# Kernel tuning notes

Measured on AMD Instinct MI355X. Metric: run time of the kernel, lower is better.

Reference implementation:

```python
import jax, jax.numpy as jnp
import numpy as np

E = 384        # number of edges
HID = 128      # hidden_dim
NH = 8         # num_heads
DH = HID // NH # head_dim = 16
NR = 64        # num_radial
CUTOFF = 10.0
AIN = 2 * DH + NR + 1  # attention MLP input dim = 97


def _xavier(key, fan_in, fan_out):
    a = np.sqrt(6.0 / (fan_in + fan_out))
    return jax.random.uniform(key, (fan_in, fan_out), jnp.float32, -a, a)


def setup_inputs() -> dict:
    key = jax.random.key(0)
    ks = jax.random.split(key, 16)
    return {
        "edge_features": jax.random.normal(ks[0], (E, HID), jnp.float32),
        "edge_coords": jax.random.normal(ks[1], (E, 3), jnp.float32),
        "edge_mask": jnp.zeros((E, E), jnp.float32),  # 0 = connected
        "wq": _xavier(ks[2], HID, HID),
        "wk": _xavier(ks[3], HID, HID),
        "wv": _xavier(ks[4], HID, HID),
        "rbf_centers": jnp.linspace(0.0, CUTOFF, NR).astype(jnp.float32),
        "rbf_widths": jnp.full((NR,), 0.5, jnp.float32),
        "a_w1": _xavier(ks[5], AIN, HID), "a_b1": jnp.zeros((HID,), jnp.float32),
        "a_w2": _xavier(ks[6], HID, HID), "a_b2": jnp.zeros((HID,), jnp.float32),
        "a_w3": _xavier(ks[7], HID, NH),  "a_b3": jnp.zeros((NH,), jnp.float32),
        "g_w1": _xavier(ks[8], DH, HID),  "g_b1": jnp.zeros((HID,), jnp.float32),
        "g_w2": _xavier(ks[9], HID, 1),   "g_b2": jnp.zeros((1,), jnp.float32),
        "wo": _xavier(ks[10], HID, HID),  "bo": jnp.zeros((HID,), jnp.float32),
        "ln_g": jnp.ones((HID,), jnp.float32),
        "ln_b": jnp.zeros((HID,), jnp.float32),
        "edge_index": jax.random.randint(ks[11], (2, E), 0, E, jnp.int64) if jax.config.jax_enable_x64 else jax.random.randint(ks[11], (2, E), 0, E, jnp.int32),
    }


def reference(edge_features, edge_coords, edge_mask,
              wq, wk, wv, rbf_centers, rbf_widths,
              a_w1, a_b1, a_w2, a_b2, a_w3, a_b3,
              g_w1, g_b1, g_w2, g_b2, wo, bo, ln_g, ln_b,
              edge_index):
    silu = jax.nn.silu
    n = edge_features.shape[0]

    q = (edge_features @ wq).reshape(n, NH, DH)
    k = (edge_features @ wk).reshape(n, NH, DH)
    v = (edge_features @ wv).reshape(n, NH, DH)

    # pairwise geometry [E, E, ...]
    coord_diff = edge_coords[:, None, :] - edge_coords[None, :, :]
    dist = jnp.linalg.norm(coord_diff, axis=-1) + 1e-8
    dist = jnp.clip(dist, 1e-8, 1e8)
    dot = jnp.clip(jnp.sum(edge_coords[:, None, :] * edge_coords[None, :, :], -1),
                   -1e8, 1e8)
    d = dist[..., None]                               # [E, E, 1]
    rbf = jnp.exp(-rbf_widths * (d - rbf_centers) ** 2) * (d <= CUTOFF).astype(jnp.float32)

    feats = []
    coords = edge_coords
    for h in range(NH):  # structural loop over fixed num_heads
        qh = jnp.broadcast_to(q[:, h, None, :], (n, n, DH))
        kh = jnp.broadcast_to(k[None, :, h, :], (n, n, DH))
        ai = jnp.concatenate([qh, kh, rbf, dot[..., None]], -1)  # [E, E, 97]
        x = silu(ai @ a_w1 + a_b1)
        x = silu(x @ a_w2 + a_b2)
        scores = (x @ a_w3 + a_b3)[:, :, h] + edge_mask
        scores = jnp.clip(scores, -1e9, 1e9)
        attn = jax.nn.softmax(scores, axis=-1)
        attn = jnp.nan_to_num(attn, nan=0.0, posinf=1.0, neginf=0.0)
        vh = v[:, h, :]
        feats.append(attn @ vh)
        # coord gate from v_head of the query edge, broadcast over keys
        gates = jax.nn.sigmoid(silu(vh @ g_w1 + g_b1) @ g_w2 + g_b2)  # [E, 1]
        coords = coords + jnp.einsum('ij,ijc->ic', attn * gates, coord_diff) / NH

    upd = jnp.concatenate(feats, -1)             # [E, hidden]
    y = edge_features + upd @ wo + bo            # residual + out_proj
    mu = jnp.mean(y, -1, keepdims=True)
    var = jnp.var(y, -1, keepdims=True)
    out_f = (y - mu) / jnp.sqrt(var + 1e-5) * ln_g + ln_b
    return out_f, coords
```

## Files before the change

kernel.cpp:

```cpp
#include <hip/hip_runtime.h>
#include <hip/hip_bf16.h>

#define N 384
#define HIDN 128
#define NHD 8
#define DHD 16
#define NRB 64
#define CUTF 10.0f

#define WS_V 0
#define WS_QPB (WS_V + N*HIDN)
#define WS_KPB (WS_QPB + N*NHD*HIDN/2)
#define WS_GATE (WS_KPB + N*NHD*HIDN/2)
#define WS_UPD (WS_GATE + N*NHD)
#define WS_SCORES (WS_UPD + N*HIDN)

typedef short bf16x8 __attribute__((ext_vector_type(8)));
typedef float floatx4 __attribute__((ext_vector_type(4)));
#define MFMA16(a, b, c) __builtin_amdgcn_mfma_f32_16x16x32_bf16(a, b, c, 0, 0, 0)

__device__ __forceinline__ float siluf(float x) { return x / (1.0f + __expf(-x)); }
__device__ __forceinline__ float silu_fast(float x) {
    return x * __builtin_amdgcn_rcpf(1.0f + __expf(-x));
}
__device__ __forceinline__ short f2bf(float f) {
    unsigned int b = __float_as_uint(f);
    unsigned int r = (b + 0x7fffu + ((b >> 16) & 1u)) >> 16;
    return (short)r;
}
__device__ __forceinline__ float bf2f(short s) {
    return __uint_as_float(((unsigned int)(unsigned short)s) << 16);
}
__device__ __forceinline__ float wave_sum(float v) {
    for (int o = 32; o; o >>= 1) v += __shfl_down(v, o, 64);
    return v;
}

__global__ __launch_bounds__(128) void k_pre(const float* __restrict__ ef,
    const float* __restrict__ wq, const float* __restrict__ wk, const float* __restrict__ wv,
    const float* __restrict__ aw1,
    const float* __restrict__ gw1, const float* __restrict__ gb1,
    const float* __restrict__ gw2, const float* __restrict__ gb2,
    float* __restrict__ v, unsigned short* __restrict__ Qpb,
    unsigned short* __restrict__ Kpb, float* __restrict__ gates) {
    __shared__ float sE[HIDN], sQ[HIDN], sK[HIDN], sV[HIDN];
    __shared__ float sRed[2];
    int i = blockIdx.x, t = threadIdx.x;
    sE[t] = ef[i * HIDN + t];
    __syncthreads();
    float aq = 0.f, ak = 0.f, av = 0.f;
#pragma unroll 8
    for (int c = 0; c < HIDN; c++) {
        float e = sE[c];
        aq += e * wq[c * HIDN + t];
        ak += e * wk[c * HIDN + t];
        av += e * wv[c * HIDN + t];
    }
    v[i * HIDN + t] = av;
    sQ[t] = aq; sK[t] = ak; sV[t] = av;
    __syncthreads();
    for (int h = 0; h < NHD; h++) {
        float accq = 0.f, acck = 0.f;
#pragma unroll
        for (int d = 0; d < DHD; d++) {
            accq += sQ[h * DHD + d] * aw1[d * HIDN + t];
            acck += sK[h * DHD + d] * aw1[(DHD + d) * HIDN + t];
        }
        Qpb[(i * NHD + h) * HIDN + t] = (unsigned short)f2bf(accq);
        Kpb[(i * NHD + h) * HIDN + t] = (unsigned short)f2bf(acck);
        float tt = gb1[t];
#pragma unroll
        for (int d = 0; d < DHD; d++) tt += sV[h * DHD + d] * gw1[d * HIDN + t];
        float contrib = siluf(tt) * gw2[t];
        float s = wave_sum(contrib);
        if ((t & 63) == 0) sRed[t >> 6] = s;
        __syncthreads();
        if (t == 0) gates[i * NHD + h] = 1.0f / (1.0f + __expf(-(sRed[0] + sRed[1] + gb2[0])));
        __syncthreads();
    }
}

#define OFF_W1RT 0
#define OFF_QPB  18432
#define OFF_W3T  20480
#define OFF_B1   24576
#define OFF_W1D  25088
#define OFF_B2   25600
#define OFF_AB3  26112
#define OFF_SDD  26144
#define OFF_RBF  26272
#define OFF_R    28576
#define SMEM_SZ  37024
#define OFF_STAGE 0

__global__ __launch_bounds__(256, 2) void k_scores_mfma(
    const float* __restrict__ coords, const float* __restrict__ mask,
    const float* __restrict__ centers, const float* __restrict__ widths,
    const float* __restrict__ aw1, const float* __restrict__ ab1,
    const float* __restrict__ aw2, const float* __restrict__ ab2,
    const float* __restrict__ aw3, const float* __restrict__ ab3,
    const unsigned short* __restrict__ Qpb, const unsigned short* __restrict__ Kpb,
    float* __restrict__ scores) {
    __shared__ __align__(16) char smem[SMEM_SZ];
    const int t = threadIdx.x;
    const int lane = t & 63;
    const int w = t >> 6;
    const int l15 = lane & 15;
    const int quad = lane >> 4;
    const int i = blockIdx.y;
    const int jb = blockIdx.x * 128;

    for (int idx = t; idx < HIDN * HIDN; idx += 256) {
        int k = idx >> 7, n = idx & 127;
        *(short*)(smem + OFF_STAGE + n * 272 + k * 2) = f2bf(aw2[idx]);
    }
    __syncthreads();
    bf16x8 BW2[8][4];
#pragma unroll
    for (int ct = 0; ct < 8; ct++)
#pragma unroll
        for (int ks = 0; ks < 4; ks++)
            BW2[ct][ks] = *(const bf16x8*)(smem + OFF_STAGE + (ct * 16 + l15) * 272 + ks * 64 + quad * 16);
    __syncthreads();
    for (int idx = t; idx < NRB * HIDN; idx += 256) {
        int r = idx >> 7, n = idx & 127;
        *(short*)(smem + OFF_W1RT + n * 144 + r * 2) = f2bf(aw1[32 * HIDN + idx]);
    }
    {
        const unsigned int* qsrc = (const unsigned int*)(Qpb + (size_t)i * NHD * HIDN);
        for (int idx = t; idx < 512; idx += 256) *(unsigned int*)(smem + OFF_QPB + idx * 4) = qsrc[idx];
    }
    for (int idx = t; idx < HIDN * NHD; idx += 256) {
        int c = idx >> 3, h = idx & 7;
        *(float*)(smem + OFF_W3T + (h * 128 + c) * 4) = aw3[idx];
    }
    if (t < 128) {
        *(float*)(smem + OFF_B1 + t * 4) = ab1[t];
        *(float*)(smem + OFF_W1D + t * 4) = aw1[96 * HIDN + t];
        *(float*)(smem + OFF_B2 + t * 4) = ab2[t];
    }
    if (t < 8) *(float*)(smem + OFF_AB3 + t * 4) = ab3[t];
    const float cix = coords[i * 3], ciy = coords[i * 3 + 1], ciz = coords[i * 3 + 2];
    __syncthreads();

    for (int ch = 0; ch < 8; ch++) {
        const int j0 = jb + ch * 16;
        {
            int r = t & 63, j4 = t >> 6;
            float cr = centers[r], rw = widths[r];
#pragma unroll
            for (int p = 0; p < 4; p++) {
                int j = j4 + p * 4;
                int jj = j0 + j;
                float jx = coords[jj * 3], jy = coords[jj * 3 + 1], jz = coords[jj * 3 + 2];
                float dx = cix - jx, dy = ciy - jy, dz = ciz - jz;
                float dist = sqrtf(dx * dx + dy * dy + dz * dz) + 1e-8f;
                dist = fminf(fmaxf(dist, 1e-8f), 1e8f);
                float dd = dist - cr;
                float val = (dist <= CUTF) ? __expf(-rw * dd * dd) : 0.0f;
                *(short*)(smem + OFF_RBF + j * 144 + r * 2) = f2bf(val);
            }
            if (t < 16) {
                int jj = j0 + t;
                float jx = coords[jj * 3], jy = coords[jj * 3 + 1], jz = coords[jj * 3 + 2];
                float dot = fminf(fmaxf(cix * jx + ciy * jy + ciz * jz, -1e8f), 1e8f);
                *(float*)(smem + OFF_SDD + t * 4) = dot;
            }
        }
        __syncthreads();
        {
            bf16x8 ra0 = *(const bf16x8*)(smem + OFF_RBF + l15 * 144 + quad * 16);
            bf16x8 ra1 = *(const bf16x8*)(smem + OFF_RBF + l15 * 144 + 64 + quad * 16);
#pragma unroll
            for (int cc = 0; cc < 2; cc++) {
                int ct = w + cc * 4;
                floatx4 acc = {0.f, 0.f, 0.f, 0.f};
                bf16x8 b0 = *(const bf16x8*)(smem + OFF_W1RT + (ct * 16 + l15) * 144 + quad * 16);
                bf16x8 b1f = *(const bf16x8*)(smem + OFF_W1RT + (ct * 16 + l15) * 144 + 64 + quad * 16);
                acc = MFMA16(ra0, b0, acc);
                acc = MFMA16(ra1, b1f, acc);
                int c = ct * 16 + l15;
                float b1v = *(const float*)(smem + OFF_B1 + c * 4);
                float w1dv = *(const float*)(smem + OFF_W1D + c * 4);
#pragma unroll
                for (int r = 0; r < 4; r++) {
                    int j = quad * 4 + r;
                    float dotv = *(const float*)(smem + OFF_SDD + j * 4);
                    *(float*)(smem + OFF_R + j * 528 + c * 4) = acc[r] + b1v + dotv * w1dv;
                }
            }
        }
        __syncthreads();
#pragma unroll
        for (int hh = 0; hh < 2; hh++) {
            const int h = hh * 4 + w;
            const unsigned short* kpr = Kpb + ((size_t)(j0 + l15) * NHD + h) * HIDN;
            bf16x8 A[4];
#pragma unroll
            for (int f = 0; f < 4; f++) {
                int c8 = f * 32 + quad * 8;
                bf16x8 kp = *(const bf16x8*)(kpr + c8);
                bf16x8 qp = *(const bf16x8*)(smem + OFF_QPB + (h * 128 + c8) * 2);
                float4 r0 = *(const float4*)(smem + OFF_R + l15 * 528 + c8 * 4);
                float4 r1 = *(const float4*)(smem + OFF_R + l15 * 528 + c8 * 4 + 16);
                float rr[8] = {r0.x, r0.y, r0.z, r0.w, r1.x, r1.y, r1.z, r1.w};
                bf16x8 a;
#pragma unroll
                for (int e = 0; e < 8; e++) {
                    float x = silu_fast(bf2f(kp[e]) + bf2f(qp[e]) + rr[e]);
                    a[e] = f2bf(x);
                }
                A[f] = a;
            }
            float part[4] = {0.f, 0.f, 0.f, 0.f};
#pragma unroll
            for (int ct = 0; ct < 8; ct++) {
                floatx4 acc = {0.f, 0.f, 0.f, 0.f};
                acc = MFMA16(A[0], BW2[ct][0], acc);
                acc = MFMA16(A[1], BW2[ct][1], acc);
                acc = MFMA16(A[2], BW2[ct][2], acc);
                acc = MFMA16(A[3], BW2[ct][3], acc);
                int c = ct * 16 + l15;
                float b2v = *(const float*)(smem + OFF_B2 + c * 4);
                float w3v = *(const float*)(smem + OFF_W3T + (h * 128 + c) * 4);
#pragma unroll
                for (int r = 0; r < 4; r++)
                    part[r] += silu_fast(acc[r] + b2v) * w3v;
            }
#pragma unroll
            for (int off = 1; off < 16; off <<= 1) {
#pragma unroll
                for (int r = 0; r < 4; r++) part[r] += __shfl_xor(part[r], off, 64);
            }
            if (l15 == 0) {
                float ab3v = *(const float*)(smem + OFF_AB3 + h * 4);
#pragma unroll
                for (int r = 0; r < 4; r++) {
                    int j = quad * 4 + r;
                    float s = part[r] + ab3v + mask[(size_t)i * N + j0 + j];
                    s = fminf(fmaxf(s, -1e9f), 1e9f);
                    scores[((size_t)h * N + i) * N + j0 + j] = s;
                }
            }
        }
        __syncthreads();
    }
}

__global__ __launch_bounds__(256) void k_attn2(
    const float* __restrict__ scores, const float* __restrict__ v,
    const float* __restrict__ gates, const float* __restrict__ coords,
    float* __restrict__ upd, float* __restrict__ out) {
    __shared__ float sA[4][N];
    __shared__ float sCrd[N * 3];
    __shared__ float sC[NHD][3];
    int i = blockIdx.x, t = threadIdx.x, w = t >> 6, lane = t & 63;
    for (int idx = t; idx < N * 3; idx += 256) sCrd[idx] = coords[idx];
    float cix = coords[i * 3], ciy = coords[i * 3 + 1], ciz = coords[i * 3 + 2];
    __syncthreads();
    for (int hh = 0; hh < 2; hh++) {
        int h = hh * 4 + w;
        const float* srow = scores + ((size_t)h * N + i) * N;
        float s[6];
#pragma unroll
        for (int p = 0; p < 6; p++) s[p] = srow[lane + 64 * p];
        float m = s[0];
#pragma unroll
        for (int p = 1; p < 6; p++) m = fmaxf(m, s[p]);
        for (int off = 1; off < 64; off <<= 1) m = fmaxf(m, __shfl_xor(m, off, 64));
        float e[6], sum = 0.f;
#pragma unroll
        for (int p = 0; p < 6; p++) { e[p] = __expf(s[p] - m); sum += e[p]; }
        for (int off = 1; off < 64; off <<= 1) sum += __shfl_xor(sum, off, 64);
        float inv = 1.0f / sum;
#pragma unroll
        for (int p = 0; p < 6; p++) sA[w][lane + 64 * p] = e[p] * inv;
        __syncthreads();
        int d4 = lane & 3, grp = lane >> 2;
        float4 f4 = {0.f, 0.f, 0.f, 0.f};
        for (int j = grp; j < N; j += 16) {
            float a = sA[w][j];
            float4 vv = *(const float4*)(v + j * HIDN + h * DHD + d4 * 4);
            f4.x += a * vv.x; f4.y += a * vv.y; f4.z += a * vv.z; f4.w += a * vv.w;
        }
#pragma unroll
        for (int off = 4; off < 64; off <<= 1) {
            f4.x += __shfl_xor(f4.x, off, 64);
            f4.y += __shfl_xor(f4.y, off, 64);
            f4.z += __shfl_xor(f4.z, off, 64);
            f4.w += __shfl_xor(f4.w, off, 64);
        }
        if (lane < 4) *(float4*)(upd + i * HIDN + h * DHD + lane * 4) = f4;
        float cx = 0.f, cy = 0.f, cz = 0.f;
#pragma unroll
        for (int p = 0; p < 6; p++) {
            int j = lane + 64 * p;
            float a = sA[w][j];
            cx += a * (cix - sCrd[j * 3]);
            cy += a * (ciy - sCrd[j * 3 + 1]);
            cz += a * (ciz - sCrd[j * 3 + 2]);
        }
        for (int off = 1; off < 64; off <<= 1) {
            cx += __shfl_xor(cx, off, 64);
            cy += __shfl_xor(cy, off, 64);
            cz += __shfl_xor(cz, off, 64);
        }
        if (lane == 0) {
            float g = gates[i * NHD + h] * (1.0f / NHD);
            sC[h][0] = g * cx; sC[h][1] = g * cy; sC[h][2] = g * cz;
        }
        __syncthreads();
    }
    if (t < 3) {
        float acc = coords[i * 3 + t];
#pragma unroll
        for (int h = 0; h < NHD; h++) acc += sC[h][t];
        out[N * HIDN + i * 3 + t] = acc;
    }
}

__global__ __launch_bounds__(128) void k_out(
    const float* __restrict__ ef, const float* __restrict__ upd,
    const float* __restrict__ wo, const float* __restrict__ bo,
    const float* __restrict__ lng, const float* __restrict__ lnb,
    float* __restrict__ out) {
    __shared__ float sU[HIDN];
    __shared__ float sR[2];
    int i = blockIdx.x, c = threadIdx.x;
    sU[c] = upd[i * HIDN + c];
    __syncthreads();
    float y = ef[i * HIDN + c] + bo[c];
#pragma unroll 8
    for (int cp = 0; cp < HIDN; cp++) y += sU[cp] * wo[cp * HIDN + c];
    float s = wave_sum(y);
    if ((c & 63) == 0) sR[c >> 6] = s;
    __syncthreads();
    float mu = (sR[0] + sR[1]) * (1.0f / HIDN);
    __syncthreads();
    float dv = y - mu;
    float s2 = wave_sum(dv * dv);
    if ((c & 63) == 0) sR[c >> 6] = s2;
    __syncthreads();
    float var = (sR[0] + sR[1]) * (1.0f / HIDN);
    out[i * HIDN + c] = dv * rsqrtf(var + 1e-5f) * lng[c] + lnb[c];
}

extern "C" void kernel_launch(void* const* d_in, const int* in_sizes, int n_in,
                              void* d_out, int out_size, void* d_ws, size_t ws_size,
                              hipStream_t stream) {
    const float* ef      = (const float*)d_in[0];
    const float* coords  = (const float*)d_in[1];
    const float* mask    = (const float*)d_in[2];
    const float* wq      = (const float*)d_in[3];
    const float* wk      = (const float*)d_in[4];
    const float* wv      = (const float*)d_in[5];
    const float* centers = (const float*)d_in[6];
    const float* widths  = (const float*)d_in[7];
    const float* aw1     = (const float*)d_in[8];
    const float* ab1     = (const float*)d_in[9];
    const float* aw2     = (const float*)d_in[10];
    const float* ab2     = (const float*)d_in[11];
    const float* aw3     = (const float*)d_in[12];
    const float* ab3     = (const float*)d_in[13];
    const float* gw1     = (const float*)d_in[14];
    const float* gb1     = (const float*)d_in[15];
    const float* gw2     = (const float*)d_in[16];
    const float* gb2     = (const float*)d_in[17];
    const float* wo      = (const float*)d_in[18];
    const float* bo      = (const float*)d_in[19];
    const float* lng     = (const float*)d_in[20];
    const float* lnb     = (const float*)d_in[21];
    float* ws = (float*)d_ws;
    float* v      = ws + WS_V;
    unsigned short* Qpb = (unsigned short*)(ws + WS_QPB);
    unsigned short* Kpb = (unsigned short*)(ws + WS_KPB);
    float* gates  = ws + WS_GATE;
    float* upd    = ws + WS_UPD;
    float* scores = ws + WS_SCORES;
    float* out = (float*)d_out;

    k_pre<<<N, 128, 0, stream>>>(ef, wq, wk, wv, aw1, gw1, gb1, gw2, gb2, v, Qpb, Kpb, gates);
    k_scores_mfma<<<dim3(3, N), 256, 0, stream>>>(
        coords, mask, centers, widths, aw1, ab1, aw2, ab2, aw3, ab3, Qpb, Kpb, scores);
    k_attn2<<<N, 256, 0, stream>>>(scores, v, gates, coords, upd, out);
    k_out<<<N, 128, 0, stream>>>(ef, upd, wo, bo, lng, lnb, out);
}
```

Before: 298.6 us.

## Restructure scores kernel to 8 waves per head with swizzled LDS weights, fuse output projection

The scores kernel now runs 512 threads, one wave per head, and keeps the W2 weights in XOR-swizzled LDS instead of per-thread registers. That frees register pressure and removes the 8x re-read of Q/R per head loop. K projections are stored in fp32 and read directly, Q is prefetched into registers, and W3 is stored as bf16. The separate output-projection/LayerNorm kernel is fused into the attention kernel, which removes one launch and the upd round trip. The trade-offs are more LDS per block, twice the global Kp traffic, and extra LDS reads of W2 in the inner loop.

Result: slower. 361.7 us (+21.1%).

```diff
diff --git a/kernel.cpp b/kernel.cpp
--- a/kernel.cpp
+++ b/kernel.cpp
@@ -9,11 +9,10 @@
 #define CUTF 10.0f
 
 #define WS_V 0
-#define WS_QPB (WS_V + N*HIDN)
-#define WS_KPB (WS_QPB + N*NHD*HIDN/2)
-#define WS_GATE (WS_KPB + N*NHD*HIDN/2)
-#define WS_UPD (WS_GATE + N*NHD)
-#define WS_SCORES (WS_UPD + N*HIDN)
+#define WS_KP (WS_V + N*HIDN)
+#define WS_QPB (WS_KP + N*NHD*HIDN)
+#define WS_GATE (WS_QPB + N*NHD*HIDN/2)
+#define WS_SCORES (WS_GATE + N*NHD)
 
 typedef short bf16x8 __attribute__((ext_vector_type(8)));
 typedef float floatx4 __attribute__((ext_vector_type(4)));
@@ -30,6 +29,11 @@
 }
 __device__ __forceinline__ float bf2f(short s) {
     return __uint_as_float(((unsigned int)(unsigned short)s) << 16);
+}
+__device__ __forceinline__ unsigned int pk_bf16(float a, float b) {
+    union { __hip_bfloat162 h; unsigned int u; } cv;
+    cv.h = __float22bfloat162_rn(make_float2(a, b));
+    return cv.u;
 }
 __device__ __forceinline__ float wave_sum(float v) {
     for (int o = 32; o; o >>= 1) v += __shfl_down(v, o, 64);
@@ -42,7 +46,7 @@
     const float* __restrict__ gw1, const float* __restrict__ gb1,
     const float* __restrict__ gw2, const float* __restrict__ gb2,
     float* __restrict__ v, unsigned short* __restrict__ Qpb,
-    unsigned short* __restrict__ Kpb, float* __restrict__ gates) {
+    float* __restrict__ Kp, float* __restrict__ gates) {
     __shared__ float sE[HIDN], sQ[HIDN], sK[HIDN], sV[HIDN];
     __shared__ float sRed[2];
     int i = blockIdx.x, t = threadIdx.x;
@@ -67,7 +71,7 @@
             acck += sK[h * DHD + d] * aw1[(DHD + d) * HIDN + t];
         }
         Qpb[(i * NHD + h) * HIDN + t] = (unsigned short)f2bf(accq);
-        Kpb[(i * NHD + h) * HIDN + t] = (unsigned short)f2bf(acck);
+        Kp[(i * NHD + h) * HIDN + t] = acck;
         float tt = gb1[t];
 #pragma unroll
         for (int d = 0; d < DHD; d++) tt += sV[h * DHD + d] * gw1[d * HIDN + t];
@@ -80,26 +84,25 @@
     }
 }
 
-#define OFF_W1RT 0
-#define OFF_QPB  18432
-#define OFF_W3T  20480
-#define OFF_B1   24576
-#define OFF_W1D  25088
-#define OFF_B2   25600
-#define OFF_AB3  26112
-#define OFF_SDD  26144
-#define OFF_RBF  26272
-#define OFF_R    28576
-#define SMEM_SZ  37024
-#define OFF_STAGE 0
-
-__global__ __launch_bounds__(256, 2) void k_scores_mfma(
+#define OFF_W2T  0
+#define OFF_W1RT 32768
+#define OFF_W3T  49152
+#define OFF_B1   51200
+#define OFF_W1D  51712
+#define OFF_B2   52224
+#define OFF_AB3  52736
+#define OFF_SDD  52768
+#define OFF_RBF  52832
+#define OFF_R    54880
+#define SMEM_SZ  63072
+
+__global__ __launch_bounds__(512, 4) void k_scores_mfma(
     const float* __restrict__ coords, const float* __restrict__ mask,
     const float* __restrict__ centers, const float* __restrict__ widths,
     const float* __restrict__ aw1, const float* __restrict__ ab1,
     const float* __restrict__ aw2, const float* __restrict__ ab2,
     const float* __restrict__ aw3, const float* __restrict__ ab3,
-    const unsigned short* __restrict__ Qpb, const unsigned short* __restrict__ Kpb,
+    const unsigned short* __restrict__ Qpb, const float* __restrict__ Kp,
     float* __restrict__ scores) {
     __shared__ __align__(16) char smem[SMEM_SZ];
     const int t = threadIdx.x;
@@ -110,29 +113,19 @@
     const int i = blockIdx.y;
     const int jb = blockIdx.x * 128;
 
-    for (int idx = t; idx < HIDN * HIDN; idx += 256) {
-        int k = idx >> 7, n = idx & 127;
-        *(short*)(smem + OFF_STAGE + n * 272 + k * 2) = f2bf(aw2[idx]);
-    }
-    __syncthreads();
-    bf16x8 BW2[8][4];
-#pragma unroll
-    for (int ct = 0; ct < 8; ct++)
-#pragma unroll
-        for (int ks = 0; ks < 4; ks++)
-            BW2[ct][ks] = *(const bf16x8*)(smem + OFF_STAGE + (ct * 16 + l15) * 272 + ks * 64 + quad * 16);
-    __syncthreads();
-    for (int idx = t; idx < NRB * HIDN; idx += 256) {
-        int r = idx >> 7, n = idx & 127;
-        *(short*)(smem + OFF_W1RT + n * 144 + r * 2) = f2bf(aw1[32 * HIDN + idx]);
-    }
-    {
-        const unsigned int* qsrc = (const unsigned int*)(Qpb + (size_t)i * NHD * HIDN);
-        for (int idx = t; idx < 512; idx += 256) *(unsigned int*)(smem + OFF_QPB + idx * 4) = qsrc[idx];
-    }
-    for (int idx = t; idx < HIDN * NHD; idx += 256) {
+    for (int idx = t; idx < 8192; idx += 512) {
+        int k2 = (idx & 63) * 2, n = idx >> 6;
+        unsigned int p = pk_bf16(aw2[k2 * HIDN + n], aw2[(k2 + 1) * HIDN + n]);
+        *(unsigned int*)(smem + OFF_W2T + n * 256 + (((k2 >> 3) ^ (n & 15)) << 4) + (k2 & 7) * 2) = p;
+    }
+    for (int idx = t; idx < 4096; idx += 512) {
+        int r2 = (idx & 31) * 2, n = idx >> 5;
+        unsigned int p = pk_bf16(aw1[(32 + r2) * HIDN + n], aw1[(33 + r2) * HIDN + n]);
+        *(unsigned int*)(smem + OFF_W1RT + n * 128 + (((r2 >> 3) ^ (n & 7)) << 4) + (r2 & 7) * 2) = p;
+    }
+    for (int idx = t; idx < HIDN * NHD; idx += 512) {
         int c = idx >> 3, h = idx & 7;
-        *(float*)(smem + OFF_W3T + (h * 128 + c) * 4) = aw3[idx];
+        *(short*)(smem + OFF_W3T + (h * 128 + c) * 2) = f2bf(aw3[idx]);
     }
     if (t < 128) {
         *(float*)(smem + OFF_B1 + t * 4) = ab1[t];
@@ -140,89 +133,100 @@
         *(float*)(smem + OFF_B2 + t * 4) = ab2[t];
     }
     if (t < 8) *(float*)(smem + OFF_AB3 + t * 4) = ab3[t];
+    bf16x8 qpf[4];
+#pragma unroll
+    for (int f = 0; f < 4; f++)
+        qpf[f] = *(const bf16x8*)(Qpb + ((size_t)i * NHD + w) * HIDN + f * 32 + quad * 8);
     const float cix = coords[i * 3], ciy = coords[i * 3 + 1], ciz = coords[i * 3 + 2];
     __syncthreads();
 
     for (int ch = 0; ch < 8; ch++) {
         const int j0 = jb + ch * 16;
         {
-            int r = t & 63, j4 = t >> 6;
+            int r = t & 63, jj = t >> 6;
             float cr = centers[r], rw = widths[r];
 #pragma unroll
-            for (int p = 0; p < 4; p++) {
-                int j = j4 + p * 4;
-                int jj = j0 + j;
-                float jx = coords[jj * 3], jy = coords[jj * 3 + 1], jz = coords[jj * 3 + 2];
+            for (int p = 0; p < 2; p++) {
+                int j = jj + p * 8;
+                int jg = j0 + j;
+                float jx = coords[jg * 3], jy = coords[jg * 3 + 1], jz = coords[jg * 3 + 2];
                 float dx = cix - jx, dy = ciy - jy, dz = ciz - jz;
                 float dist = sqrtf(dx * dx + dy * dy + dz * dz) + 1e-8f;
                 dist = fminf(fmaxf(dist, 1e-8f), 1e8f);
                 float dd = dist - cr;
                 float val = (dist <= CUTF) ? __expf(-rw * dd * dd) : 0.0f;
-                *(short*)(smem + OFF_RBF + j * 144 + r * 2) = f2bf(val);
+                *(short*)(smem + OFF_RBF + j * 128 + (((r >> 3) ^ (j & 7)) << 4) + (r & 7) * 2) = f2bf(val);
             }
             if (t < 16) {
-                int jj = j0 + t;
-                float jx = coords[jj * 3], jy = coords[jj * 3 + 1], jz = coords[jj * 3 + 2];
+                int jg = j0 + t;
+                float jx = coords[jg * 3], jy = coords[jg * 3 + 1], jz = coords[jg * 3 + 2];
                 float dot = fminf(fmaxf(cix * jx + ciy * jy + ciz * jz, -1e8f), 1e8f);
                 *(float*)(smem + OFF_SDD + t * 4) = dot;
             }
         }
         __syncthreads();
         {
-            bf16x8 ra0 = *(const bf16x8*)(smem + OFF_RBF + l15 * 144 + quad * 16);
-            bf16x8 ra1 = *(const bf16x8*)(smem + OFF_RBF + l15 * 144 + 64 + quad * 16);
-#pragma unroll
-            for (int cc = 0; cc < 2; cc++) {
-                int ct = w + cc * 4;
-                floatx4 acc = {0.f, 0.f, 0.f, 0.f};
-                bf16x8 b0 = *(const bf16x8*)(smem + OFF_W1RT + (ct * 16 + l15) * 144 + quad * 16);
-                bf16x8 b1f = *(const bf16x8*)(smem + OFF_W1RT + (ct * 16 + l15) * 144 + 64 + quad * 16);
-                acc = MFMA16(ra0, b0, acc);
-                acc = MFMA16(ra1, b1f, acc);
-                int c = ct * 16 + l15;
-                float b1v = *(const float*)(smem + OFF_B1 + c * 4);
-                float w1dv = *(const float*)(smem + OFF_W1D + c * 4);
-#pragma unroll
-                for (int r = 0; r < 4; r++) {
-                    int j = quad * 4 + r;
-                    float dotv = *(const float*)(smem + OFF_SDD + j * 4);
-                    *(float*)(smem + OFF_R + j * 528 + c * 4) = acc[r] + b1v + dotv * w1dv;
-                }
-            }
-        }
-        __syncthreads();
-#pragma unroll
-        for (int hh = 0; hh < 2; hh++) {
-            const int h = hh * 4 + w;
-            const unsigned short* kpr = Kpb + ((size_t)(j0 + l15) * NHD + h) * HIDN;
+            bf16x8 ra0 = *(const bf16x8*)(smem + OFF_RBF + l15 * 128 + (((quad) ^ (l15 & 7)) << 4));
+            bf16x8 ra1 = *(const bf16x8*)(smem + OFF_RBF + l15 * 128 + (((quad + 4) ^ (l15 & 7)) << 4));
+            int n = w * 16 + l15;
+            bf16x8 b0 = *(const bf16x8*)(smem + OFF_W1RT + n * 128 + (((quad) ^ (n & 7)) << 4));
+            bf16x8 b1 = *(const bf16x8*)(smem + OFF_W1RT + n * 128 + (((quad + 4) ^ (n & 7)) << 4));
+            floatx4 acc = {0.f, 0.f, 0.f, 0.f};
+            acc = MFMA16(ra0, b0, acc);
+            acc = MFMA16(ra1, b1, acc);
+            float b1v = *(const float*)(smem + OFF_B1 + n * 4);
+            float w1dv = *(const float*)(smem + OFF_W1D + n * 4);
+            int gc = n >> 2;
+#pragma unroll
+            for (int r = 0; r < 4; r++) {
+                int j = quad * 4 + r;
+                float dotv = *(const float*)(smem + OFF_SDD + j * 4);
+                *(float*)(smem + OFF_R + j * 512 + ((gc ^ j) << 4) + (n & 3) * 4) = acc[r] + b1v + dotv * w1dv;
+            }
+        }
+        __syncthreads();
+        {
+            const float* kpr = Kp + ((size_t)(j0 + l15) * NHD + w) * HIDN;
             bf16x8 A[4];
 #pragma unroll
             for (int f = 0; f < 4; f++) {
                 int c8 = f * 32 + quad * 8;
-                bf16x8 kp = *(const bf16x8*)(kpr + c8);
-                bf16x8 qp = *(const bf16x8*)(smem + OFF_QPB + (h * 128 + c8) * 2);
-                float4 r0 = *(const float4*)(smem + OFF_R + l15 * 528 + c8 * 4);
-                float4 r1 = *(const float4*)(smem + OFF_R + l15 * 528 + c8 * 4 + 16);
-                float rr[8] = {r0.x, r0.y, r0.z, r0.w, r1.x, r1.y, r1.z, r1.w};
-                bf16x8 a;
-#pragma unroll
-                for (int e = 0; e < 8; e++) {
-                    float x = silu_fast(bf2f(kp[e]) + bf2f(qp[e]) + rr[e]);
-                    a[e] = f2bf(x);
-                }
-                A[f] = a;
+                float4 kp0 = *(const float4*)(kpr + c8);
+                float4 kp1 = *(const float4*)(kpr + c8 + 4);
+                int g0 = f * 8 + quad * 2;
+                float4 r0 = *(const float4*)(smem + OFF_R + l15 * 512 + (((g0) ^ l15) << 4));
+                float4 r1 = *(const float4*)(smem + OFF_R + l15 * 512 + (((g0 + 1) ^ l15) << 4));
+                float x0 = silu_fast(kp0.x + bf2f(qpf[f][0]) + r0.x);
+                float x1 = silu_fast(kp0.y + bf2f(qpf[f][1]) + r0.y);
+                float x2 = silu_fast(kp0.z + bf2f(qpf[f][2]) + r0.z);
+                float x3 = silu_fast(kp0.w + bf2f(qpf[f][3]) + r0.w);
+                float x4 = silu_fast(kp1.x + bf2f(qpf[f][4]) + r1.x);
+                float x5 = silu_fast(kp1.y + bf2f(qpf[f][5]) + r1.y);
+                float x6 = silu_fast(kp1.z + bf2f(qpf[f][6]) + r1.z);
+                float x7 = silu_fast(kp1.w + bf2f(qpf[f][7]) + r1.w);
+                union { int4 i4; bf16x8 v; } u;
+                u.i4.x = (int)pk_bf16(x0, x1);
+                u.i4.y = (int)pk_bf16(x2, x3);
+                u.i4.z = (int)pk_bf16(x4, x5);
+                u.i4.w = (int)pk_bf16(x6, x7);
+                A[f] = u.v;
             }
             float part[4] = {0.f, 0.f, 0.f, 0.f};
 #pragma unroll
             for (int ct = 0; ct < 8; ct++) {
+                const char* wb = smem + OFF_W2T + (ct * 16 + l15) * 256;
+                bf16x8 b0 = *(const bf16x8*)(wb + (((quad) ^ l15) << 4));
+                bf16x8 b1 = *(const bf16x8*)(wb + (((quad + 4) ^ l15) << 4));
+                bf16x8 b2 = *(const bf16x8*)(wb + (((quad + 8) ^ l15) << 4));
+                bf16x8 b3 = *(const bf16x8*)(wb + (((quad + 12) ^ l15) << 4));
                 floatx4 acc = {0.f, 0.f, 0.f, 0.f};
-                acc = MFMA16(A[0], BW2[ct][0], acc);
-                acc = MFMA16(A[1], BW2[ct][1], acc);
-                acc = MFMA16(A[2], BW2[ct][2], acc);
-                acc = MFMA16(A[3], BW2[ct][3], acc);
+                acc = MFMA16(A[0], b0, acc);
+                acc = MFMA16(A[1], b1, acc);
+                acc = MFMA16(A[2], b2, acc);
+                acc = MFMA16(A[3], b3, acc);
                 int c = ct * 16 + l15;
                 float b2v = *(const float*)(smem + OFF_B2 + c * 4);
-                float w3v = *(const float*)(smem + OFF_W3T + (h * 128 + c) * 4);
+                float w3v = bf2f(*(const short*)(smem + OFF_W3T + (w * 128 + c) * 2));
 #pragma unroll
                 for (int r = 0; r < 4; r++)
                     part[r] += silu_fast(acc[r] + b2v) * w3v;
@@ -233,13 +237,13 @@
                 for (int r = 0; r < 4; r++) part[r] += __shfl_xor(part[r], off, 64);
             }
             if (l15 == 0) {
-                float ab3v = *(const float*)(smem + OFF_AB3 + h * 4);
+                float ab3v = *(const float*)(smem + OFF_AB3 + w * 4);
 #pragma unroll
                 for (int r = 0; r < 4; r++) {
                     int j = quad * 4 + r;
                     float s = part[r] + ab3v + mask[(size_t)i * N + j0 + j];
                     s = fminf(fmaxf(s, -1e9f), 1e9f);
-                    scores[((size_t)h * N + i) * N + j0 + j] = s;
+                    scores[((size_t)w * N + i) * N + j0 + j] = s;
                 }
             }
         }
@@ -247,13 +251,18 @@
     }
 }
 
-__global__ __launch_bounds__(256) void k_attn2(
+__global__ __launch_bounds__(256) void k_attn_out(
     const float* __restrict__ scores, const float* __restrict__ v,
     const float* __restrict__ gates, const float* __restrict__ coords,
-    float* __restrict__ upd, float* __restrict__ out) {
+    const float* __restrict__ ef, const float* __restrict__ wo,
+    const float* __restrict__ bo, const float* __restrict__ lng,
+    const float* __restrict__ lnb, float* __restrict__ out) {
     __shared__ float sA[4][N];
     __shared__ float sCrd[N * 3];
     __shared__ float sC[NHD][3];
+    __shared__ float sUpd[HIDN];
+    __shared__ float sYp[2][HIDN];
+    __shared__ float sR[2], sR2[2];
     int i = blockIdx.x, t = threadIdx.x, w = t >> 6, lane = t & 63;
     for (int idx = t; idx < N * 3; idx += 256) sCrd[idx] = coords[idx];
     float cix = coords[i * 3], ciy = coords[i * 3 + 1], ciz = coords[i * 3 + 2];
@@ -290,7 +299,7 @@
             f4.z += __shfl_xor(f4.z, off, 64);
             f4.w += __shfl_xor(f4.w, off, 64);
         }
-        if (lane < 4) *(float4*)(upd + i * HIDN + h * DHD + lane * 4) = f4;
+        if (lane < 4) *(float4*)(sUpd + h * DHD + lane * 4) = f4;
         float cx = 0.f, cy = 0.f, cz = 0.f;
 #pragma unroll
         for (int p = 0; p < 6; p++) {
@@ -311,38 +320,39 @@
         }
         __syncthreads();
     }
+    {
+        int c = t & 127, half = t >> 7;
+        float acc = 0.f;
+#pragma unroll 8
+        for (int cp = half * 64; cp < half * 64 + 64; cp++)
+            acc += sUpd[cp] * wo[cp * HIDN + c];
+        sYp[half][c] = acc;
+    }
+    __syncthreads();
+    float y = 0.f, dv = 0.f;
+    if (t < 128) {
+        y = ef[i * HIDN + t] + bo[t] + sYp[0][t] + sYp[1][t];
+        float s = wave_sum(y);
+        if ((t & 63) == 0) sR[t >> 6] = s;
+    }
+    __syncthreads();
+    if (t < 128) {
+        float mu = (sR[0] + sR[1]) * (1.0f / HIDN);
+        dv = y - mu;
+        float s2 = wave_sum(dv * dv);
+        if ((t & 63) == 0) sR2[t >> 6] = s2;
+    }
+    __syncthreads();
+    if (t < 128) {
+        float var = (sR2[0] + sR2[1]) * (1.0f / HIDN);
+        out[i * HIDN + t] = dv * rsqrtf(var + 1e-5f) * lng[t] + lnb[t];
+    }
     if (t < 3) {
         float acc = coords[i * 3 + t];
 #pragma unroll
         for (int h = 0; h < NHD; h++) acc += sC[h][t];
         out[N * HIDN + i * 3 + t] = acc;
     }
-}
-
-__global__ __launch_bounds__(128) void k_out(
-    const float* __restrict__ ef, const float* __restrict__ upd,
-    const float* __restrict__ wo, const float* __restrict__ bo,
-    const float* __restrict__ lng, const float* __restrict__ lnb,
-    float* __restrict__ out) {
-    __shared__ float sU[HIDN];
-    __shared__ float sR[2];
-    int i = blockIdx.x, c = threadIdx.x;
-    sU[c] = upd[i * HIDN + c];
-    __syncthreads();
-    float y = ef[i * HIDN + c] + bo[c];
-#pragma unroll 8
-    for (int cp = 0; cp < HIDN; cp++) y += sU[cp] * wo[cp * HIDN + c];
-    float s = wave_sum(y);
-    if ((c & 63) == 0) sR[c >> 6] = s;
-    __syncthreads();
-    float mu = (sR[0] + sR[1]) * (1.0f / HIDN);
-    __syncthreads();
-    float dv = y - mu;
-    float s2 = wave_sum(dv * dv);
-    if ((c & 63) == 0) sR[c >> 6] = s2;
-    __syncthreads();
-    float var = (sR[0] + sR[1]) * (1.0f / HIDN);
-    out[i * HIDN + c] = dv * rsqrtf(var + 1e-5f) * lng[c] + lnb[c];
 }
 
 extern "C" void kernel_launch(void* const* d_in, const int* in_sizes, int n_in,
@@ -372,16 +382,14 @@
     const float* lnb     = (const float*)d_in[21];
     float* ws = (float*)d_ws;
     float* v      = ws + WS_V;
+    float* Kp     = ws + WS_KP;
     unsigned short* Qpb = (unsigned short*)(ws + WS_QPB);
-    unsigned short* Kpb = (unsigned short*)(ws + WS_KPB);
     float* gates  = ws + WS_GATE;
-    float* upd    = ws + WS_UPD;
     float* scores = ws + WS_SCORES;
     float* out = (float*)d_out;
 
-    k_pre<<<N, 128, 0, stream>>>(ef, wq, wk, wv, aw1, gw1, gb1, gw2, gb2, v, Qpb, Kpb, gates);
-    k_scores_mfma<<<dim3(3, N), 256, 0, stream>>>(
-        coords, mask, centers, widths, aw1, ab1, aw2, ab2, aw3, ab3, Qpb, Kpb, scores);
-    k_attn2<<<N, 256, 0, stream>>>(scores, v, gates, coords, upd, out);
-    k_out<<<N, 128, 0, stream>>>(ef, upd, wo, bo, lng, lnb, out);
-}
+    k_pre<<<N, 128, 0, stream>>>(ef, wq, wk, wv, aw1, gw1, gb1, gw2, gb2, v, Qpb, Kp, gates);
+    k_scores_mfma<<<dim3(3, N), 512, 0, stream>>>(
+        coords, mask, centers, widths, aw1, ab1, aw2, ab2, aw3, ab3, Qpb, Kp, scores);
+    k_attn_out<<<N, 256, 0, stream>>>(scores, v, gates, coords, ef, wo, bo, lng, lnb, out);
+}
```
